# Optimization experiments

Hardware: AMD Instinct MI355X
Metric: run time of the kernel (lower is better)

Reference implementation:

```python
import jax, jax.numpy as jnp
import numpy as np

A, B, T, N, C = 8, 4, 1024, 4, 2048
EPS = 1e-5
SINKHORN_ITERS = 20


def setup_inputs() -> dict:
    key = jax.random.key(0)
    ks = jax.random.split(key, 8)
    nC = N * C
    # identity-ish init per module, with small random alphas to exercise all paths
    p = 1.0 / N
    inv_sig = float(np.log(p) - np.log(1.0 - p))
    return {
        "x": jax.random.normal(ks[0], (B, T, N, C), dtype=jnp.float32),
        "output": jax.random.normal(ks[1], (B, T, C), dtype=jnp.float32),
        "input_norm_weight": jnp.ones((A, nC), dtype=jnp.float32),
        "phi_pre": 0.02 * jax.random.normal(ks[2], (A, nC, N), dtype=jnp.float32),
        "phi_post": 0.02 * jax.random.normal(ks[3], (A, nC, N), dtype=jnp.float32),
        "phi_res": 0.02 * jax.random.normal(ks[4], (A, nC, N * N), dtype=jnp.float32),
        "b_pre": jnp.full((A, N), inv_sig, dtype=jnp.float32),
        "b_post": jnp.zeros((A, N), dtype=jnp.float32),
        "b_res": jnp.broadcast_to(10.0 * jnp.eye(N, dtype=jnp.float32), (A, N, N)),
        "alpha_pre": 0.1 * jax.random.normal(ks[5], (A,), dtype=jnp.float32),
        "alpha_post": 0.1 * jax.random.normal(ks[6], (A,), dtype=jnp.float32),
        "alpha_res": 0.1 * jax.random.normal(ks[7], (A,), dtype=jnp.float32),
        "adapter_indices": jax.random.randint(jax.random.fold_in(key, 99), (B,), 0, A, dtype=jnp.int32),
    }


def sinkhorn_knopp(logits, iters):
    # logits: (B,T,n,n) -> doubly-stochastic M via alternating row/col normalization
    M = jnp.exp(logits)
    for _ in range(iters):
        M = M / M.sum(axis=-1, keepdims=True)
        M = M / M.sum(axis=-2, keepdims=True)
    return M


def reference(x, output, input_norm_weight, phi_pre, phi_post, phi_res,
              b_pre, b_post, b_res, alpha_pre, alpha_post, alpha_res,
              adapter_indices):
    Bs, Ts, n, Cc = x.shape
    idx = adapter_indices
    # per-sample adapter gather
    w = input_norm_weight[idx]                      # (B, n*C)
    x_flat = x.reshape(Bs, Ts, n * Cc)              # (B, T, n*C)
    rms = jnp.sqrt(jnp.mean(x_flat * x_flat, axis=-1, keepdims=True) + EPS)
    x_norm = w[:, None, :] * x_flat / rms           # (B, T, n*C)
    # pre gating
    pre_logits = jnp.einsum('btf,bfn->btn', x_norm, phi_pre[idx])
    H_pre = jax.nn.sigmoid(alpha_pre[idx][:, None, None] * pre_logits + b_pre[idx][:, None, :])
    x_agg = jnp.einsum('btn,btnc->btc', H_pre, x)   # (B, T, C)
    # post gating
    post_logits = jnp.einsum('btf,bfn->btn', x_norm, phi_post[idx])
    H_post = 2.0 * jax.nn.sigmoid(alpha_post[idx][:, None, None] * post_logits + b_post[idx][:, None, :])
    # residual mixing matrix via Sinkhorn
    res_logits = jnp.einsum('btf,bfm->btm', x_norm, phi_res[idx]).reshape(Bs, Ts, n, n)
    tilde_res = alpha_res[idx][:, None, None, None] * res_logits + b_res[idx][:, None, :, :]
    M = sinkhorn_knopp(tilde_res, SINKHORN_ITERS)   # (B, T, n, n)
    x_mixed = jnp.einsum('btij,btjc->btic', M, x)   # (B, T, n, C)
    y_dist = H_post[..., None] * output[:, :, None, :]
    out = x_mixed + y_dist                          # (B, T, n, C)
    return x_agg, out
```

## Files before the change

### kernel.cpp

```cpp
#include <hip/hip_runtime.h>

#define EPS 1e-5f
#define TOKS 4096
#define NCF 8192
#define CCH 2048

#define PHI_BYTES ((size_t)8 * 32 * 8192 * 2)
#define GATES_OFF PHI_BYTES
#define WS_NEED   (GATES_OFF + (size_t)TOKS * 32 * 4)

typedef __attribute__((ext_vector_type(8))) short bf16x8;
typedef __attribute__((ext_vector_type(4))) float f32x4;

__device__ __forceinline__ unsigned short f2bf(float f) {
  unsigned int u = __float_as_uint(f);
  u += 0x7FFFu + ((u >> 16) & 1u);
  return (unsigned short)(u >> 16);
}
__device__ __forceinline__ float bf2f(unsigned short s) {
  return __uint_as_float(((unsigned int)s) << 16);
}

__global__ __launch_bounds__(256)
void prep_phiT(const float* __restrict__ pre, const float* __restrict__ post,
               const float* __restrict__ res, const float* __restrict__ wnorm,
               unsigned short* __restrict__ phiT) {
  const int gid = blockIdx.x * 256 + threadIdx.x;
  const int a = gid >> 15;
  const int r = (gid >> 10) & 31;
  const int f = (gid & 1023) * 8;
  const float4 wA = *(const float4*)(wnorm + (size_t)a * NCF + f);
  const float4 wB = *(const float4*)(wnorm + (size_t)a * NCF + f + 4);
  const float wv[8] = { wA.x, wA.y, wA.z, wA.w, wB.x, wB.y, wB.z, wB.w };
  unsigned int w[4];
  #pragma unroll
  for (int p = 0; p < 4; ++p) {
    float v0 = 0.f, v1 = 0.f;
    const int e0 = f + 2 * p, e1 = f + 2 * p + 1;
    if (r < 4) {
      v0 = pre[((size_t)a * NCF + e0) * 4 + r];
      v1 = pre[((size_t)a * NCF + e1) * 4 + r];
    } else if (r < 8) {
      v0 = post[((size_t)a * NCF + e0) * 4 + (r - 4)];
      v1 = post[((size_t)a * NCF + e1) * 4 + (r - 4)];
    } else if (r < 24) {
      v0 = res[((size_t)a * NCF + e0) * 16 + (r - 8)];
      v1 = res[((size_t)a * NCF + e1) * 16 + (r - 8)];
    }
    v0 *= wv[2 * p];
    v1 *= wv[2 * p + 1];
    w[p] = (unsigned int)f2bf(v0) | ((unsigned int)f2bf(v1) << 16);
  }
  *(uint4*)(phiT + ((size_t)a * 32 + r) * NCF + f) = make_uint4(w[0], w[1], w[2], w[3]);
}

__global__ __launch_bounds__(512, 2)
void logits_gates(const float* __restrict__ x,
                  const unsigned short* __restrict__ phiT,
                  const float* __restrict__ b_pre, const float* __restrict__ b_post,
                  const float* __restrict__ b_res,
                  const float* __restrict__ a_pre, const float* __restrict__ a_post,
                  const float* __restrict__ a_res,
                  const int* __restrict__ aidx_arr,
                  float* __restrict__ gates) {
  __shared__ unsigned short xs[8][16 * 264];
  __shared__ float logits_s[8][16][32];
  __shared__ float ssq_s[8][16];

  const int tid = threadIdx.x;
  const int wave = tid >> 6, lane = tid & 63;
  const int tok0 = blockIdx.x * 16;
  const int aidx = aidx_arr[tok0 >> 10];
  const int kbase = wave * 1024;

  const float* xbase = x + (size_t)tok0 * NCF + kbase + lane * 4;
  const unsigned short* pBbase =
      phiT + ((size_t)aidx * 32 + (lane & 15)) * NCF + kbase + (lane >> 4) * 8;

  f32x4 acc0 = {0.f, 0.f, 0.f, 0.f};
  f32x4 acc1 = {0.f, 0.f, 0.f, 0.f};
  float ssq[16];
  #pragma unroll
  for (int r = 0; r < 16; ++r) ssq[r] = 0.f;

  float4 xa[16], xb[16];
  #pragma unroll
  for (int r = 0; r < 16; ++r) xa[r] = *(const float4*)(xbase + (size_t)r * NCF);
  #pragma unroll
  for (int r = 0; r < 16; ++r) xb[r] = *(const float4*)(xbase + (size_t)r * NCF + 256);

  #pragma unroll
  for (int t = 0; t < 4; ++t) {
    #pragma unroll
    for (int r = 0; r < 16; ++r) {
      const float4 v = (t & 1) ? xb[r] : xa[r];
      ssq[r] += v.x * v.x + v.y * v.y + v.z * v.z + v.w * v.w;
      *(ushort4*)&xs[wave][r * 264 + lane * 4] =
          make_ushort4(f2bf(v.x), f2bf(v.y), f2bf(v.z), f2bf(v.w));
      if (t < 2) {
        const float4 nv = *(const float4*)(xbase + (size_t)r * NCF + (t + 2) * 256);
        if (t & 1) xb[r] = nv; else xa[r] = nv;
      }
    }
    const unsigned short* pB = pBbase + t * 256;
    #pragma unroll
    for (int s = 0; s < 8; ++s) {
      bf16x8 a = *(const bf16x8*)&xs[wave][(lane & 15) * 264 + s * 32 + (lane >> 4) * 8];
      bf16x8 b0 = *(const bf16x8*)(pB + s * 32);
      bf16x8 b1 = *(const bf16x8*)(pB + 16 * NCF + s * 32);
      acc0 = __builtin_amdgcn_mfma_f32_16x16x32_bf16(a, b0, acc0, 0, 0, 0);
      acc1 = __builtin_amdgcn_mfma_f32_16x16x32_bf16(a, b1, acc1, 0, 0, 0);
    }
  }

  #pragma unroll
  for (int r = 0; r < 16; ++r) {
    float v = ssq[r];
    #pragma unroll
    for (int m = 1; m <= 32; m <<= 1) v += __shfl_xor(v, m, 64);
    if (lane == 0) ssq_s[wave][r] = v;
  }
  #pragma unroll
  for (int i = 0; i < 4; ++i) {
    logits_s[wave][(lane >> 4) * 4 + i][lane & 15] = acc0[i];
    logits_s[wave][(lane >> 4) * 4 + i][16 + (lane & 15)] = acc1[i];
  }
  __syncthreads();

  if (tid < 256) {
    const int tok = tid >> 4, cl = tid & 15;
    float L0 = 0.f, L16 = 0.f, ssqt = 0.f;
    #pragma unroll
    for (int w = 0; w < 8; ++w) {
      L0 += logits_s[w][tok][cl];
      L16 += logits_s[w][tok][16 + cl];
      ssqt += ssq_s[w][tok];
    }
    const float invr = rsqrtf(ssqt * (1.f / NCF) + EPS);

    float* g = gates + (size_t)(tok0 + tok) * 32;
    if (cl < 4) {
      const float zp = a_pre[aidx] * L0 * invr + b_pre[(size_t)aidx * 4 + cl];
      g[cl] = 1.f / (1.f + __expf(-zp));
    } else if (cl < 8) {
      const float zq = a_post[aidx] * L0 * invr + b_post[(size_t)aidx * 4 + (cl - 4)];
      g[cl] = 2.f / (1.f + __expf(-zq));
    }
    const float resv = __shfl_xor((cl & 8) ? L0 : L16, 8, 64);
    const float tl = a_res[aidx] * resv * invr + b_res[(size_t)aidx * 16 + cl];
    float m = __expf(tl);
    #pragma unroll
    for (int it = 0; it < 20; ++it) {
      float rs = m;
      rs += __shfl_xor(rs, 1, 64);
      rs += __shfl_xor(rs, 2, 64);
      m *= __builtin_amdgcn_rcpf(rs);
      float cs = m;
      cs += __shfl_xor(cs, 4, 64);
      cs += __shfl_xor(cs, 8, 64);
      m *= __builtin_amdgcn_rcpf(cs);
    }
    g[8 + cl] = m;
  }
}

__global__ __launch_bounds__(256)
void out_pass(const float* __restrict__ x, const float* __restrict__ outp,
              const float* __restrict__ gates,
              float* __restrict__ agg, float* __restrict__ big) {
  const int tok = blockIdx.x;
  const int tid = threadIdx.x;
  const float* g = gates + (size_t)tok * 32;
  float hp[4], hq[4], M[16];
  #pragma unroll
  for (int i = 0; i < 4; ++i) { hp[i] = g[i]; hq[i] = g[4 + i]; }
  #pragma unroll
  for (int i = 0; i < 16; ++i) M[i] = g[8 + i];

  const float* xrow = x + (size_t)tok * NCF;
  const float* orow = outp + (size_t)tok * CCH;
  float* arow = agg + (size_t)tok * CCH;
  float* brow = big + (size_t)tok * NCF;

  #pragma unroll
  for (int rep = 0; rep < 2; ++rep) {
    const int c = rep * 1024 + tid * 4;
    float4 xv[4];
    #pragma unroll
    for (int j = 0; j < 4; ++j) xv[j] = *(const float4*)(xrow + j * CCH + c);
    const float4 ov = *(const float4*)(orow + c);

    f32x4 ag;
    ag.x = hp[0]*xv[0].x + hp[1]*xv[1].x + hp[2]*xv[2].x + hp[3]*xv[3].x;
    ag.y = hp[0]*xv[0].y + hp[1]*xv[1].y + hp[2]*xv[2].y + hp[3]*xv[3].y;
    ag.z = hp[0]*xv[0].z + hp[1]*xv[1].z + hp[2]*xv[2].z + hp[3]*xv[3].z;
    ag.w = hp[0]*xv[0].w + hp[1]*xv[1].w + hp[2]*xv[2].w + hp[3]*xv[3].w;
    __builtin_nontemporal_store(ag, (f32x4*)(arow + c));

    #pragma unroll
    for (int i = 0; i < 4; ++i) {
      const float m0 = M[i*4+0], m1 = M[i*4+1], m2 = M[i*4+2], m3 = M[i*4+3];
      f32x4 o;
      o.x = m0*xv[0].x + m1*xv[1].x + m2*xv[2].x + m3*xv[3].x + hq[i]*ov.x;
      o.y = m0*xv[0].y + m1*xv[1].y + m2*xv[2].y + m3*xv[3].y + hq[i]*ov.y;
      o.z = m0*xv[0].z + m1*xv[1].z + m2*xv[2].z + m3*xv[3].z + hq[i]*ov.z;
      o.w = m0*xv[0].w + m1*xv[1].w + m2*xv[2].w + m3*xv[3].w + hq[i]*ov.w;
      __builtin_nontemporal_store(o, (f32x4*)(brow + i * CCH + c));
    }
  }
}

__global__ __launch_bounds__(256, 4)
void lora_fused(const float* __restrict__ x, const float* __restrict__ outp,
                const float* __restrict__ wnorm, const float* __restrict__ phi_pre,
                const float* __restrict__ phi_post, const float* __restrict__ phi_res,
                const float* __restrict__ b_pre, const float* __restrict__ b_post,
                const float* __restrict__ b_res, const float* __restrict__ a_pre,
                const float* __restrict__ a_post, const float* __restrict__ a_res,
                const int* __restrict__ aidx_arr, float* __restrict__ agg_out,
                float* __restrict__ big_out) {
  __shared__ unsigned short xsb[2][NCF];
  __shared__ float scratch[4][52];
  __shared__ float red[52];
  __shared__ float Hpre[2][4], Hpost[2][4], Msm[2][16];
  const int tid = threadIdx.x;
  const int tok0 = blockIdx.x * 2;
  const int aidx = aidx_arr[tok0 >> 10];
  const float* xr0 = x + (size_t)tok0 * NCF;
  const float* xr1 = xr0 + NCF;
  const float* wr = wnorm + (size_t)aidx * NCF;
  const float* pp = phi_pre + (size_t)aidx * NCF * 4;
  const float* pq = phi_post + (size_t)aidx * NCF * 4;
  const float* pr = phi_res + (size_t)aidx * NCF * 16;
  float acc[50];
  #pragma unroll
  for (int i = 0; i < 50; ++i) acc[i] = 0.f;
  for (int k = 0; k < 8; ++k) {
    const int f0 = (k * 256 + tid) * 4;
    const float4 w4 = *(const float4*)(wr + f0);
    const float4 xa = *(const float4*)(xr0 + f0);
    const float4 xb = *(const float4*)(xr1 + f0);
    acc[0] += xa.x*xa.x + xa.y*xa.y + xa.z*xa.z + xa.w*xa.w;
    acc[25] += xb.x*xb.x + xb.y*xb.y + xb.z*xb.z + xb.w*xb.w;
    float xw0[4] = { xa.x*w4.x, xa.y*w4.y, xa.z*w4.z, xa.w*w4.w };
    float xw1[4] = { xb.x*w4.x, xb.y*w4.y, xb.z*w4.z, xb.w*w4.w };
    *(ushort4*)&xsb[0][f0] = make_ushort4(f2bf(xa.x), f2bf(xa.y), f2bf(xa.z), f2bf(xa.w));
    *(ushort4*)&xsb[1][f0] = make_ushort4(f2bf(xb.x), f2bf(xb.y), f2bf(xb.z), f2bf(xb.w));
    #pragma unroll
    for (int d = 0; d < 4; ++d) {
      const int f = f0 + d;
      const float a0 = xw0[d], a1 = xw1[d];
      float col[24];
      const float4 P = *(const float4*)(pp + ((size_t)f << 2));
      const float4 Q = *(const float4*)(pq + ((size_t)f << 2));
      const float4 R0 = *(const float4*)(pr + ((size_t)f << 4));
      const float4 R1 = *(const float4*)(pr + ((size_t)f << 4) + 4);
      const float4 R2 = *(const float4*)(pr + ((size_t)f << 4) + 8);
      const float4 R3 = *(const float4*)(pr + ((size_t)f << 4) + 12);
      col[0]=P.x; col[1]=P.y; col[2]=P.z; col[3]=P.w;
      col[4]=Q.x; col[5]=Q.y; col[6]=Q.z; col[7]=Q.w;
      col[8]=R0.x; col[9]=R0.y; col[10]=R0.z; col[11]=R0.w;
      col[12]=R1.x; col[13]=R1.y; col[14]=R1.z; col[15]=R1.w;
      col[16]=R2.x; col[17]=R2.y; col[18]=R2.z; col[19]=R2.w;
      col[20]=R3.x; col[21]=R3.y; col[22]=R3.z; col[23]=R3.w;
      #pragma unroll
      for (int c = 0; c < 24; ++c) { acc[1 + c] += a0 * col[c]; acc[26 + c] += a1 * col[c]; }
    }
  }
  #pragma unroll
  for (int m = 1; m <= 32; m <<= 1) {
    #pragma unroll
    for (int v = 0; v < 50; ++v) acc[v] += __shfl_xor(acc[v], m, 64);
  }
  const int wave = tid >> 6, lane = tid & 63;
  if (lane == 0) {
    #pragma unroll
    for (int v = 0; v < 50; ++v) scratch[wave][v] = acc[v];
  }
  __syncthreads();
  if (tid < 50) red[tid] = scratch[0][tid] + scratch[1][tid] + scratch[2][tid] + scratch[3][tid];
  __syncthreads();
  if (tid < 32) {
    const int t = tid >> 4, l = tid & 15;
    const float invr = rsqrtf(red[t * 25] * (1.f / NCF) + EPS);
    const float tl = a_res[aidx] * red[t * 25 + 1 + 8 + l] * invr + b_res[(size_t)aidx * 16 + l];
    float m = __expf(tl);
    #pragma unroll
    for (int it = 0; it < 20; ++it) {
      float rs = m; rs += __shfl_xor(rs, 1, 64); rs += __shfl_xor(rs, 2, 64);
      m *= __builtin_amdgcn_rcpf(rs);
      float cs = m; cs += __shfl_xor(cs, 4, 64); cs += __shfl_xor(cs, 8, 64);
      m *= __builtin_amdgcn_rcpf(cs);
    }
    Msm[t][l] = m;
  } else if (tid < 40) {
    const int q = tid - 32, t = q >> 2, n = q & 3;
    const float invr = rsqrtf(red[t * 25] * (1.f / NCF) + EPS);
    const float zp = a_pre[aidx] * red[t * 25 + 1 + n] * invr + b_pre[(size_t)aidx * 4 + n];
    const float zq = a_post[aidx] * red[t * 25 + 1 + 4 + n] * invr + b_post[(size_t)aidx * 4 + n];
    Hpre[t][n] = 1.f / (1.f + __expf(-zp));
    Hpost[t][n] = 2.f / (1.f + __expf(-zq));
  }
  __syncthreads();
  #pragma unroll
  for (int t = 0; t < 2; ++t) {
    const int tok = tok0 + t;
    const float* orow = outp + (size_t)tok * CCH;
    float* arow = agg_out + (size_t)tok * CCH;
    float* brow = big_out + (size_t)tok * 4 * CCH;
    const float hp0 = Hpre[t][0], hp1 = Hpre[t][1], hp2 = Hpre[t][2], hp3 = Hpre[t][3];
    float Mr[16];
    #pragma unroll
    for (int i = 0; i < 16; ++i) Mr[i] = Msm[t][i];
    const float hq[4] = { Hpost[t][0], Hpost[t][1], Hpost[t][2], Hpost[t][3] };
    #pragma unroll
    for (int w = 0; w < 2; ++w) {
      const int c0 = (w * 256 + tid) * 4;
      float4 xv[4];
      #pragma unroll
      for (int n = 0; n < 4; ++n) {
        const ushort4 u = *(const ushort4*)&xsb[t][n * CCH + c0];
        xv[n] = make_float4(bf2f(u.x), bf2f(u.y), bf2f(u.z), bf2f(u.w));
      }
      const float4 ov = *(const float4*)(orow + c0);
      float4 ag;
      ag.x = hp0*xv[0].x + hp1*xv[1].x + hp2*xv[2].x + hp3*xv[3].x;
      ag.y = hp0*xv[0].y + hp1*xv[1].y + hp2*xv[2].y + hp3*xv[3].y;
      ag.z = hp0*xv[0].z + hp1*xv[1].z + hp2*xv[2].z + hp3*xv[3].z;
      ag.w = hp0*xv[0].w + hp1*xv[1].w + hp2*xv[2].w + hp3*xv[3].w;
      *(float4*)(arow + c0) = ag;
      #pragma unroll
      for (int i = 0; i < 4; ++i) {
        const float m0 = Mr[i*4+0], m1 = Mr[i*4+1], m2 = Mr[i*4+2], m3 = Mr[i*4+3];
        float4 o;
        o.x = m0*xv[0].x + m1*xv[1].x + m2*xv[2].x + m3*xv[3].x + hq[i]*ov.x;
        o.y = m0*xv[0].y + m1*xv[1].y + m2*xv[2].y + m3*xv[3].y + hq[i]*ov.y;
        o.z = m0*xv[0].z + m1*xv[1].z + m2*xv[2].z + m3*xv[3].z + hq[i]*ov.z;
        o.w = m0*xv[0].w + m1*xv[1].w + m2*xv[2].w + m3*xv[3].w + hq[i]*ov.w;
        *(float4*)(brow + (size_t)i * CCH + c0) = o;
      }
    }
  }
}

extern "C" void kernel_launch(void* const* d_in, const int* in_sizes, int n_in,
                              void* d_out, int out_size, void* d_ws, size_t ws_size,
                              hipStream_t stream) {
  const float* x     = (const float*)d_in[0];
  const float* outp  = (const float*)d_in[1];
  const float* wnorm = (const float*)d_in[2];
  const float* ppre  = (const float*)d_in[3];
  const float* ppost = (const float*)d_in[4];
  const float* pres  = (const float*)d_in[5];
  const float* bpre  = (const float*)d_in[6];
  const float* bpost = (const float*)d_in[7];
  const float* bres  = (const float*)d_in[8];
  const float* apre  = (const float*)d_in[9];
  const float* apost = (const float*)d_in[10];
  const float* ares  = (const float*)d_in[11];
  const int*   aidx  = (const int*)d_in[12];

  float* agg = (float*)d_out;
  float* big = (float*)d_out + (size_t)TOKS * CCH;

  if (ws_size >= WS_NEED) {
    unsigned short* phiT = (unsigned short*)d_ws;
    float* gates = (float*)((char*)d_ws + GATES_OFF);
    hipLaunchKernelGGL(prep_phiT, dim3(1024), dim3(256), 0, stream,
                       ppre, ppost, pres, wnorm, phiT);
    hipLaunchKernelGGL(logits_gates, dim3(256), dim3(512), 0, stream,
                       x, phiT, bpre, bpost, bres, apre, apost, ares, aidx, gates);
    hipLaunchKernelGGL(out_pass, dim3(4096), dim3(256), 0, stream, x, outp, gates, agg, big);
  } else {
    hipLaunchKernelGGL(lora_fused, dim3(2048), dim3(256), 0, stream,
                       x, outp, wnorm, ppre, ppost, pres,
                       bpre, bpost, bres, apre, apost, ares, aidx, agg, big);
  }
}
```

Baseline: 110.5 us.

## Stream x tiles directly to LDS with double-buffered async loads in logits kernel

The logits kernel now uses global_load_lds to copy fp32 x chunks directly into a swizzled, double-buffered LDS area per wave, overlapping the next chunk's load with MFMA work on the current one. This replaces the register-staged loads and bf16 conversion stores. The bf16 conversion and sum of squares move to the LDS read side. Cross-wave reduction now uses LDS atomics into a single accumulator instead of per-wave arrays plus a serial sum. Launch bounds drop the 2-blocks hint, and LDS use grows to about 128KB, which likely limits occupancy to one block per CU.

```diff
diff --git a/kernel.cpp b/kernel.cpp
--- a/kernel.cpp
+++ b/kernel.cpp
@@ -19,6 +19,12 @@
 }
 __device__ __forceinline__ float bf2f(unsigned short s) {
   return __uint_as_float(((unsigned int)s) << 16);
+}
+
+__device__ __forceinline__ void gload16(const float* g, float* l) {
+  __builtin_amdgcn_global_load_lds(
+      (const __attribute__((address_space(1))) void*)g,
+      (__attribute__((address_space(3))) void*)l, 16, 0, 0);
 }
 
 __global__ __launch_bounds__(256)
@@ -54,7 +60,7 @@
   *(uint4*)(phiT + ((size_t)a * 32 + r) * NCF + f) = make_uint4(w[0], w[1], w[2], w[3]);
 }
 
-__global__ __launch_bounds__(512, 2)
+__global__ __launch_bounds__(512)
 void logits_gates(const float* __restrict__ x,
                   const unsigned short* __restrict__ phiT,
                   const float* __restrict__ b_pre, const float* __restrict__ b_post,
@@ -63,9 +69,9 @@
                   const float* __restrict__ a_res,
                   const int* __restrict__ aidx_arr,
                   float* __restrict__ gates) {
-  __shared__ unsigned short xs[8][16 * 264];
-  __shared__ float logits_s[8][16][32];
-  __shared__ float ssq_s[8][16];
+  __shared__ float xsf[8][2][2048];
+  __shared__ float logAcc[16][32];
+  __shared__ float ssqAcc[16];
 
   const int tid = threadIdx.x;
   const int wave = tid >> 6, lane = tid & 63;
@@ -73,81 +79,97 @@
   const int aidx = aidx_arr[tok0 >> 10];
   const int kbase = wave * 1024;
 
-  const float* xbase = x + (size_t)tok0 * NCF + kbase + lane * 4;
+  ((float*)logAcc)[tid & 511] = 0.f;
+  if (tid < 16) ssqAcc[tid] = 0.f;
+  __syncthreads();
+
+  const int jr0 = lane >> 5;
+  const int lb  = lane & 31;
+  const int rrow = lane & 15;
+  const int lbase = ((lane >> 4) * 2) ^ (rrow & 7);
+  const int rowoff = rrow * 128;
+
   const unsigned short* pBbase =
-      phiT + ((size_t)aidx * 32 + (lane & 15)) * NCF + kbase + (lane >> 4) * 8;
+      phiT + ((size_t)aidx * 32 + rrow) * NCF + kbase + (lane >> 4) * 8;
 
   f32x4 acc0 = {0.f, 0.f, 0.f, 0.f};
   f32x4 acc1 = {0.f, 0.f, 0.f, 0.f};
-  float ssq[16];
-  #pragma unroll
-  for (int r = 0; r < 16; ++r) ssq[r] = 0.f;
-
-  float4 xa[16], xb[16];
-  #pragma unroll
-  for (int r = 0; r < 16; ++r) xa[r] = *(const float4*)(xbase + (size_t)r * NCF);
-  #pragma unroll
-  for (int r = 0; r < 16; ++r) xb[r] = *(const float4*)(xbase + (size_t)r * NCF + 256);
-
-  #pragma unroll
-  for (int t = 0; t < 4; ++t) {
-    #pragma unroll
-    for (int r = 0; r < 16; ++r) {
-      const float4 v = (t & 1) ? xb[r] : xa[r];
-      ssq[r] += v.x * v.x + v.y * v.y + v.z * v.z + v.w * v.w;
-      *(ushort4*)&xs[wave][r * 264 + lane * 4] =
-          make_ushort4(f2bf(v.x), f2bf(v.y), f2bf(v.z), f2bf(v.w));
-      if (t < 2) {
-        const float4 nv = *(const float4*)(xbase + (size_t)r * NCF + (t + 2) * 256);
-        if (t & 1) xb[r] = nv; else xa[r] = nv;
-      }
-    }
-    const unsigned short* pB = pBbase + t * 256;
-    #pragma unroll
-    for (int s = 0; s < 8; ++s) {
-      bf16x8 a = *(const bf16x8*)&xs[wave][(lane & 15) * 264 + s * 32 + (lane >> 4) * 8];
+  float ssql = 0.f;
+
+  #define ISSUE(c, buf)                                                          \
+    {                                                                            \
+      float* ldsb = &xsf[wave][(buf)][0];                                        \
+      _Pragma("unroll")                                                          \
+      for (int j = 0; j < 8; ++j) {                                              \
+        const int rr = 2 * j + jr0;                                              \
+        const int gb = lb ^ (rr & 7);                                            \
+        const float* gsrc =                                                      \
+            x + (size_t)(tok0 + rr) * NCF + kbase + (c) * 128 + gb * 4;          \
+        gload16(gsrc, ldsb + j * 256);                                           \
+      }                                                                          \
+    }
+
+  ISSUE(0, 0)
+  ISSUE(1, 1)
+
+  #pragma unroll
+  for (int c = 0; c < 8; ++c) {
+    if (c < 7) { asm volatile("s_waitcnt vmcnt(8)" ::: "memory"); }
+    else       { asm volatile("s_waitcnt vmcnt(0)" ::: "memory"); }
+
+    const float* lbp = &xsf[wave][c & 1][0];
+    const unsigned short* pB = pBbase + c * 128;
+    #pragma unroll
+    for (int s = 0; s < 4; ++s) {
+      const int blk0 = (s * 8) | lbase;
+      const float4 v0 = *(const float4*)(lbp + rowoff + blk0 * 4);
+      const float4 v1 = *(const float4*)(lbp + rowoff + (blk0 ^ 1) * 4);
+      ssql += v0.x*v0.x + v0.y*v0.y + v0.z*v0.z + v0.w*v0.w
+            + v1.x*v1.x + v1.y*v1.y + v1.z*v1.z + v1.w*v1.w;
+      bf16x8 a;
+      a[0] = (short)f2bf(v0.x); a[1] = (short)f2bf(v0.y);
+      a[2] = (short)f2bf(v0.z); a[3] = (short)f2bf(v0.w);
+      a[4] = (short)f2bf(v1.x); a[5] = (short)f2bf(v1.y);
+      a[6] = (short)f2bf(v1.z); a[7] = (short)f2bf(v1.w);
       bf16x8 b0 = *(const bf16x8*)(pB + s * 32);
       bf16x8 b1 = *(const bf16x8*)(pB + 16 * NCF + s * 32);
       acc0 = __builtin_amdgcn_mfma_f32_16x16x32_bf16(a, b0, acc0, 0, 0, 0);
       acc1 = __builtin_amdgcn_mfma_f32_16x16x32_bf16(a, b1, acc1, 0, 0, 0);
     }
-  }
-
-  #pragma unroll
-  for (int r = 0; r < 16; ++r) {
-    float v = ssq[r];
-    #pragma unroll
-    for (int m = 1; m <= 32; m <<= 1) v += __shfl_xor(v, m, 64);
-    if (lane == 0) ssq_s[wave][r] = v;
+    asm volatile("s_waitcnt lgkmcnt(0)" ::: "memory");
+    if (c < 6) ISSUE(c + 2, c & 1)
+  }
+  #undef ISSUE
+
+  {
+    float v = ssql;
+    v += __shfl_xor(v, 16, 64);
+    v += __shfl_xor(v, 32, 64);
+    if (lane < 16) atomicAdd(&ssqAcc[rrow], v);
   }
   #pragma unroll
   for (int i = 0; i < 4; ++i) {
-    logits_s[wave][(lane >> 4) * 4 + i][lane & 15] = acc0[i];
-    logits_s[wave][(lane >> 4) * 4 + i][16 + (lane & 15)] = acc1[i];
+    atomicAdd(&logAcc[(lane >> 4) * 4 + i][lane & 15], acc0[i]);
+    atomicAdd(&logAcc[(lane >> 4) * 4 + i][16 + (lane & 15)], acc1[i]);
   }
   __syncthreads();
 
   if (tid < 256) {
     const int tok = tid >> 4, cl = tid & 15;
-    float L0 = 0.f, L16 = 0.f, ssqt = 0.f;
-    #pragma unroll
-    for (int w = 0; w < 8; ++w) {
-      L0 += logits_s[w][tok][cl];
-      L16 += logits_s[w][tok][16 + cl];
-      ssqt += ssq_s[w][tok];
-    }
+    const float Lg   = logAcc[tok][cl];
+    const float Lres = logAcc[tok][8 + cl];
+    const float ssqt = ssqAcc[tok];
     const float invr = rsqrtf(ssqt * (1.f / NCF) + EPS);
 
     float* g = gates + (size_t)(tok0 + tok) * 32;
     if (cl < 4) {
-      const float zp = a_pre[aidx] * L0 * invr + b_pre[(size_t)aidx * 4 + cl];
+      const float zp = a_pre[aidx] * Lg * invr + b_pre[(size_t)aidx * 4 + cl];
       g[cl] = 1.f / (1.f + __expf(-zp));
     } else if (cl < 8) {
-      const float zq = a_post[aidx] * L0 * invr + b_post[(size_t)aidx * 4 + (cl - 4)];
+      const float zq = a_post[aidx] * Lg * invr + b_post[(size_t)aidx * 4 + (cl - 4)];
       g[cl] = 2.f / (1.f + __expf(-zq));
     }
-    const float resv = __shfl_xor((cl & 8) ? L0 : L16, 8, 64);
-    const float tl = a_res[aidx] * resv * invr + b_res[(size_t)aidx * 16 + cl];
+    const float tl = a_res[aidx] * Lres * invr + b_res[(size_t)aidx * 16 + cl];
     float m = __expf(tl);
     #pragma unroll
     for (int it = 0; it < 20; ++it) {
```

Result: no change. 109.9 us (-0.5%).
